# Kernel tuning notes

Hardware: AMD Instinct MI355X
Metric: run time of the kernel (lower is better)

The kernel has to match this reference:

```python
import jax, jax.numpy as jnp
import numpy as np

FRAME_LENGTH = 2048
HOP_LENGTH = 512


def setup_inputs() -> dict:
    key = jax.random.key(0)
    # (batch, num_channels, samples): 8 clips, stereo, 30 s @ 16 kHz
    x = jax.random.normal(key, (8, 2, 480000), dtype=jnp.float32)
    return {"x": x}


def reference(x):
    """Faithful Enframe.forward.

    The original applies a Conv1d whose weight is the identity matrix
    torch.eye(FL)[:, None, :] with stride=hop, per channel, then concatenates
    channel results along dim=1. Mathematically out[b, n*FL + k, t] =
    x[b, n, t*hop + k]. We implement it as a strided gather (the efficient
    form of the same math).
    """
    B, C, S = x.shape
    FL, HOP = FRAME_LENGTH, HOP_LENGTH
    T = (S - FL) // HOP + 1  # frames_num = 934 for S=480000
    # gather_idx[k, t] = t*HOP + k  -> (FL, T)
    gather_idx = jnp.arange(FL)[:, None] + jnp.arange(T)[None, :] * HOP
    frames = x[:, :, gather_idx]  # (B, C, FL, T)
    # torch.cat over channel dim puts channel-major blocks of size FL on dim 1
    return frames.reshape(B, C * FL, T)
```

## Files before the change

kernel.cpp:

```cpp
#include <hip/hip_runtime.h>


constexpr int FL  = 2048;
constexpr int HOP = 512;

__global__ __launch_bounds__(256)
void enframe_kernel(const float* __restrict__ x, float* __restrict__ out,
                    int S, int T) {
    const int bc = blockIdx.x;
    const int g  = blockIdx.y & 127;
    const int tt = blockIdx.y >> 7;
    const int t  = tt * 256 + threadIdx.x;
    if (t >= T) return;

    const float4* xp = (const float4*)(x + (size_t)bc * S + (size_t)t * HOP + (size_t)g * 16);
    float4 v0 = xp[0];
    float4 v1 = xp[1];
    float4 v2 = xp[2];
    float4 v3 = xp[3];

    float* op = out + ((size_t)bc * FL + (size_t)g * 16) * T + t;
    float vals[16] = {v0.x, v0.y, v0.z, v0.w,
                      v1.x, v1.y, v1.z, v1.w,
                      v2.x, v2.y, v2.z, v2.w,
                      v3.x, v3.y, v3.z, v3.w};
#pragma unroll
    for (int j = 0; j < 16; ++j)
        __builtin_nontemporal_store(vals[j], op + (size_t)j * T);
}

extern "C" void kernel_launch(void* const* d_in, const int* in_sizes, int n_in,
                              void* d_out, int out_size, void* d_ws, size_t ws_size,
                              hipStream_t stream) {
    const float* x = (const float*)d_in[0];
    float* out = (float*)d_out;
    const int BC = 16;
    const int S  = in_sizes[0] / BC;
    const int T  = (S - FL) / HOP + 1;
    const int t_tiles = (T + 255) / 256;
    dim3 grid(BC, (unsigned)(t_tiles * 128));
    enframe_kernel<<<grid, 256, 0, stream>>>(x, out, S, T);
}
```

Measured before the change: 169.2 us.

## Stage overlapping frame rows in LDS to reuse input across hop offsets

Each block now loads a tile of 67 hop-rows by 64 samples into padded shared memory, then writes four output rows per loaded element. This uses the fact that frames overlap by a factor of four (FL/HOP). Input is read once per tile instead of once per frame, which cuts redundant global reads. The cost is an LDS round trip and a __syncthreads, and the output writes stay strided across T.

```diff
diff --git a/kernel.cpp b/kernel.cpp
--- a/kernel.cpp
+++ b/kernel.cpp
@@ -3,30 +3,56 @@
 
 constexpr int FL  = 2048;
 constexpr int HOP = 512;
+constexpr int TT  = 64;
+constexpr int RT  = 64;
+constexpr int ROWS = TT + 3;
+constexpr int LSTR = RT + 1;
 
 __global__ __launch_bounds__(256)
 void enframe_kernel(const float* __restrict__ x, float* __restrict__ out,
                     int S, int T) {
+    __shared__ float lds[ROWS * LSTR];
+
     const int bc = blockIdx.x;
-    const int g  = blockIdx.y & 127;
-    const int tt = blockIdx.y >> 7;
-    const int t  = tt * 256 + threadIdx.x;
-    if (t >= T) return;
+    const int t0 = blockIdx.y * TT;
+    const int r0 = blockIdx.z * RT;
+    const int tid = threadIdx.x;
 
-    const float4* xp = (const float4*)(x + (size_t)bc * S + (size_t)t * HOP + (size_t)g * 16);
-    float4 v0 = xp[0];
-    float4 v1 = xp[1];
-    float4 v2 = xp[2];
-    float4 v3 = xp[3];
+    {
+        const int rg   = tid & 15;
+        const int row0 = tid >> 4;
+        const float* xb = x + (size_t)bc * S;
+#pragma unroll
+        for (int p = 0; p < 5; ++p) {
+            const int row = p * 16 + row0;
+            if (row < ROWS) {
+                const int trow = t0 + row;
+                if ((size_t)trow * HOP + r0 + RT <= (size_t)S) {
+                    const float4 v = *(const float4*)(xb + (size_t)trow * HOP + r0 + rg * 4);
+                    float* l = lds + row * LSTR + rg * 4;
+                    l[0] = v.x; l[1] = v.y; l[2] = v.z; l[3] = v.w;
+                }
+            }
+        }
+    }
+    __syncthreads();
 
-    float* op = out + ((size_t)bc * FL + (size_t)g * 16) * T + t;
-    float vals[16] = {v0.x, v0.y, v0.z, v0.w,
-                      v1.x, v1.y, v1.z, v1.w,
-                      v2.x, v2.y, v2.z, v2.w,
-                      v3.x, v3.y, v3.z, v3.w};
+    const int t_local = tid & 63;
+    const int idx     = tid >> 6;
+    const int t       = t0 + t_local;
+    if (t < T) {
+        float* ob = out + (size_t)bc * FL * T + t;
 #pragma unroll
-    for (int j = 0; j < 16; ++j)
-        __builtin_nontemporal_store(vals[j], op + (size_t)j * T);
+        for (int rb = 0; rb < RT; rb += 4) {
+            const int rr = rb + idx;
+            const int k0 = r0 + rr;
+#pragma unroll
+            for (int h = 0; h < 4; ++h) {
+                const float v = lds[(t_local + h) * LSTR + rr];
+                __builtin_nontemporal_store(v, ob + (size_t)(h * HOP + k0) * T);
+            }
+        }
+    }
 }
 
 extern "C" void kernel_launch(void* const* d_in, const int* in_sizes, int n_in,
@@ -37,7 +63,8 @@
     const int BC = 16;
     const int S  = in_sizes[0] / BC;
     const int T  = (S - FL) / HOP + 1;
-    const int t_tiles = (T + 255) / 256;
-    dim3 grid(BC, (unsigned)(t_tiles * 128));
+    const int t_tiles = (T + TT - 1) / TT;
+    const int r_tiles = HOP / RT;
+    dim3 grid(BC, (unsigned)t_tiles, (unsigned)r_tiles);
     enframe_kernel<<<grid, 256, 0, stream>>>(x, out, S, T);
 }
```

New measurement: 177.0 us. 1.05x slower.
